# Kernel tuning notes

Hardware: AMD Instinct MI355X
Metric: run time of the kernel (lower is better)

Reference implementation:

```python
import jax, jax.numpy as jnp
import numpy as np

B, N, D, E = 64, 512, 256, 128   # batch, n_nodes, node_model_dim, edge_model_dim
N_ITERS = 20                      # max_iter_sinkhorn with fixed_n_iters=True


def setup_inputs() -> dict:
    key = jax.random.key(0)
    ks = jax.random.split(key, 9)
    return {
        "node_embeddings_inputs": jax.random.normal(ks[0], (B, N, D), jnp.float32),
        "node_masks_inputs": jax.random.randint(ks[1], (B, N), 0, 2).astype(bool),
        "node_embeddings_outputs": jax.random.normal(ks[2], (B, N, D), jnp.float32),
        # learned parameters
        "node_padding_features": jax.random.normal(ks[3], (1, 1, D), jnp.float32),
        "positional_encoding_outputs": jax.random.normal(ks[4], (1, N, D), jnp.float32),
        # stand-in for the (externally defined) EvoformerSetMatching pair stack:
        # a bilinear pair-affinity head, followed by the module's own linear_aff
        "W_a": jax.random.normal(ks[5], (D, E), jnp.float32) / np.sqrt(D),
        "W_b": jax.random.normal(ks[6], (D, E), jnp.float32) / np.sqrt(D),
        "w_aff": jax.random.normal(ks[7], (E,), jnp.float32) / np.sqrt(E),  # linear_aff weight
        "b_aff": jnp.zeros((), jnp.float32),                                # linear_aff bias
    }


def _sinkhorn(K, n_iters):
    # Fixed-iteration Sinkhorn projection toward a doubly-stochastic matrix:
    # alternately normalize columns (dim=2 sums) and rows (dim=1 sums).
    def step(P, _):
        P = P / jnp.sum(P, axis=2, keepdims=True)  # row-normalize over inputs axis
        P = P / jnp.sum(P, axis=1, keepdims=True)  # col-normalize over outputs axis
        return P, None
    P, _ = jax.lax.scan(step, K, None, length=n_iters)
    return P


def reference(node_embeddings_inputs, node_masks_inputs, node_embeddings_outputs,
              node_padding_features, positional_encoding_outputs,
              W_a, W_b, w_aff, b_aff):
    # replace padded input nodes with the learned padding feature
    mask = node_masks_inputs[..., None]                              # [B, N, 1]
    x_in = jnp.where(mask, node_padding_features, node_embeddings_inputs)
    # add positional encoding to output nodes (add_positionnal_outputs=True)
    x_out = node_embeddings_outputs + positional_encoding_outputs

    # pairwise affinity: aff[b, i(out), j(in)]  (linear_aff fused into the contraction
    # so the [B,N,N,E] pair tensor is never materialized)
    a = (x_out @ W_a) * w_aff                                        # [B, N, E]
    b = x_in @ W_b                                                   # [B, N, E]
    aff = jnp.einsum('bie,bje->bij', a, b) + b_aff                   # [B, N, N]

    # approximate doubly-stochastic init: average of the two marginal softmaxes
    K = 0.5 * jax.nn.softmax(aff, axis=1) + 0.5 * jax.nn.softmax(aff, axis=2)
    return _sinkhorn(K, N_ITERS)
```

## Files before the change

### kernel.cpp

```cpp
#include <hip/hip_runtime.h>
#include <cstddef>

static constexpr int CB = 64;
static constexpr int CN = 512;
static constexpr int CD = 256;
static constexpr int CE = 128;
static constexpr int CIT = 20;

typedef _Float16 half_t;
typedef __attribute__((ext_vector_type(8))) _Float16 v8h;
typedef __attribute__((ext_vector_type(4))) _Float16 v4h;
typedef __attribute__((ext_vector_type(4))) float v4f;

__device__ __forceinline__ void llc_store4(v4f* p, v4f v) {
  asm volatile("global_store_dwordx4 %0, %1, off sc0 sc1"
               :: "v"(p), "v"(v) : "memory");
}
__device__ __forceinline__ void llc_load3x4(const v4f* p0, const v4f* p1,
                                            const v4f* p2,
                                            v4f& a, v4f& b, v4f& c) {
  asm volatile("global_load_dwordx4 %0, %3, off sc0 sc1\n\t"
               "global_load_dwordx4 %1, %4, off sc0 sc1\n\t"
               "global_load_dwordx4 %2, %5, off sc0 sc1\n\t"
               "s_waitcnt vmcnt(0)"
               : "=&v"(a), "=&v"(b), "=&v"(c)
               : "v"(p0), "v"(p1), "v"(p2)
               : "memory");
}

__global__ __launch_bounds__(512) void k0_init(
    const void* __restrict__ mask, int* __restrict__ flag,
    const float* __restrict__ W_a, const float* __restrict__ W_b,
    const float* __restrict__ w_aff,
    half_t* __restrict__ WaF, half_t* __restrict__ WbF,
    float4* __restrict__ clearp, int nclear4) {
  const int tid = threadIdx.x;
  const int blk = blockIdx.x;
  if (blk == 1) return;
  if (blk >= 18) {
    const int idx = (blk - 18) * 512 + tid;
    if (idx < nclear4)
      clearp[idx] = make_float4(-1.0f, -1.0f, -1.0f, -1.0f);
    return;
  }
  if (blk >= 2) {
    const bool is_a = (blk < 10);
    const float* W = is_a ? W_a : W_b;
    half_t* WF = is_a ? WaF : WbF;
    const int e = (blk - (is_a ? 2 : 10)) * 512 + tid;
    const int fB = e >> 6, lane = e & 63;
    const int nn = fB >> 3, kf = fB & 7;
    const int col = nn * 16 + (lane & 15);
    const int q = lane >> 4;
    const float scale = is_a ? w_aff[col] : 1.0f;
    v8h hv;
#pragma unroll
    for (int j = 0; j < 8; ++j) {
      const int k = kf * 32 + q * 8 + j;
      hv[j] = (half_t)(W[(size_t)k * CE + col] * scale);
    }
    *(v8h*)&WF[(size_t)e * 8] = hv;
    return;
  }
  __shared__ int cnt[5];
  if (tid < 5) cnt[tid] = 0;
  __syncthreads();
  const unsigned char* p = (const unsigned char*)mask;
  int l0 = 0, l1 = 0, l2 = 0, l3 = 0, l4 = 0;
  const int base = tid * 64;
  for (int k = 0; k < 64; ++k) {
    const int off = base + k;
    if (p[off]) {
      const int m4 = off & 3;
      if (m4 == 1) l1++;
      else if (m4 == 2) l2++;
      else if (m4 == 3) l3++;
      else if ((off & 7) == 4) l4++;
      else l0++;
    }
  }
  if (l0) atomicAdd(&cnt[0], 1);
  if (l1) atomicAdd(&cnt[1], 1);
  if (l2) atomicAdd(&cnt[2], 1);
  if (l3) atomicAdd(&cnt[3], 1);
  if (l4) atomicAdd(&cnt[4], 1);
  __syncthreads();
  if (tid == 0) {
    int f;
    if (cnt[1]) f = 1;
    else if (cnt[2] || cnt[3]) f = 2;
    else if (cnt[4]) f = 0;
    else if (cnt[0]) f = 3;
    else f = 1;
    *flag = f;
  }
}

__global__ __launch_bounds__(256) void prep_both(
    const float* __restrict__ out_emb, const float* __restrict__ pos,
    const float* __restrict__ in_emb, const float* __restrict__ pad,
    const void* __restrict__ maskp, const int* __restrict__ flagp,
    const half_t* __restrict__ WaF, const half_t* __restrict__ WbF,
    half_t* __restrict__ A_h, half_t* __restrict__ Bm_h) {
  __shared__ half_t Xs[64][264];
  const int tid = threadIdx.x;
  const int wv = tid >> 6, ln = tid & 63;
  const bool isA = blockIdx.x < 512;
  const int row0 = (isA ? blockIdx.x : blockIdx.x - 512) * 64;
  const float* X = isA ? out_emb : in_emb;
  const float* extra = isA ? pos : pad;
  const half_t* Wfrag = isA ? WaF : WbF;
  half_t* out = isA ? A_h : Bm_h;
  const int flag = isA ? 0 : *flagp;

#pragma unroll 4
  for (int it = 0; it < 16; ++it) {
    const int r = it * 4 + wv;
    const int row = row0 + r;
    const int c = ln * 4;
    float4 x4;
    if (isA) {
      x4 = *(const float4*)&X[(size_t)row * CD + c];
      const int i = row & (CN - 1);
      const float4 p4 = *(const float4*)&extra[(size_t)i * CD + c];
      x4.x += p4.x; x4.y += p4.y; x4.z += p4.z; x4.w += p4.w;
    } else {
      bool m;
      if (flag == 1)      m = ((const unsigned char*)maskp)[row] != 0;
      else if (flag == 2) m = ((const float*)maskp)[row] != 0.0f;
      else if (flag == 3) m = ((const long long*)maskp)[row] != 0;
      else                m = ((const int*)maskp)[row] != 0;
      if (m) x4 = *(const float4*)&extra[c];
      else   x4 = *(const float4*)&X[(size_t)row * CD + c];
    }
    v4h hv;
    hv[0] = (half_t)x4.x; hv[1] = (half_t)x4.y;
    hv[2] = (half_t)x4.z; hv[3] = (half_t)x4.w;
    *(v4h*)&Xs[r][c] = hv;
  }
  __syncthreads();

  const int q = ln >> 4, l = ln & 15;
  v8h af[8];
#pragma unroll
  for (int kf = 0; kf < 8; ++kf)
    af[kf] = *(v8h*)&Xs[wv * 16 + l][kf * 32 + q * 8];
  v4f acc[8] = {};
#pragma unroll
  for (int nn = 0; nn < 8; ++nn) {
    v8h bf[8];
#pragma unroll
    for (int kf = 0; kf < 8; ++kf)
      bf[kf] = *(const v8h*)&Wfrag[(size_t)((nn * 8 + kf) * 64 + ln) * 8];
#pragma unroll
    for (int kf = 0; kf < 8; ++kf)
      acc[nn] = __builtin_amdgcn_mfma_f32_16x16x32_f16(af[kf], bf[kf], acc[nn], 0, 0, 0);
  }
#pragma unroll
  for (int nn = 0; nn < 8; ++nn)
#pragma unroll
    for (int g = 0; g < 4; ++g) {
      const int row = row0 + wv * 16 + q * 4 + g;
      out[(size_t)row * CE + nn * 16 + l] = (half_t)acc[nn][g];
    }
}

__global__ __launch_bounds__(512, 2) void fused_reg(
    const half_t* __restrict__ A_h, const half_t* __restrict__ B_h,
    const float* __restrict__ baff, float* __restrict__ P,
    float* __restrict__ partInit, float* __restrict__ partIter) {
  __shared__ float comb2[8][512][2];
  __shared__ __align__(16) float2 w12[512];
  __shared__ __align__(16) float QsL[512];
  __shared__ __align__(16) v4f csinv4[128];
  __shared__ half_t w1h[512];
  __shared__ half_t w2h[512];

  const int tid = threadIdx.x;
  const int wv = tid >> 6, ln = tid & 63;
  const int q = ln >> 4, l = ln & 15;
  const int b = blockIdx.x & 63;
  const int slab = blockIdx.x >> 6;
  const int i0 = slab * 128;
  const float bbs = *baff - 2.7725887f;

  int rs3[3];
  {
    int k = 0;
#pragma unroll
    for (int sl = 0; sl < 4; ++sl)
      if (sl != slab) rs3[k++] = sl;
  }

  v8h af[4];
  {
    const half_t* Arow = &A_h[((size_t)b * CN + i0 + wv * 16 + l) * CE];
#pragma unroll
    for (int ki = 0; ki < 4; ++ki)
      af[ki] = *(const v8h*)&Arow[ki * 32 + q * 8];
  }
  v4h eh[32];
  v4h ehT[32];
  const half_t* Bbase = &B_h[(size_t)b * CN * CE];
#pragma unroll
  for (int ct = 0; ct < 32; ++ct) {
    v8h bf[4];
    const half_t* Brow = &Bbase[(size_t)(ct * 16 + l) * CE];
#pragma unroll
    for (int ki = 0; ki < 4; ++ki)
      bf[ki] = *(const v8h*)&Brow[ki * 32 + q * 8];
    v4f acc = {}, accT = {};
#pragma unroll
    for (int ki = 0; ki < 4; ++ki) {
      acc  = __builtin_amdgcn_mfma_f32_16x16x32_f16(af[ki], bf[ki], acc,  0, 0, 0);
      accT = __builtin_amdgcn_mfma_f32_16x16x32_f16(bf[ki], af[ki], accT, 0, 0, 0);
    }
#pragma unroll
    for (int g = 0; g < 4; ++g) {
      eh[ct][g]  = (half_t)__expf(acc[g]  + bbs);
      ehT[ct][g] = (half_t)__expf(accT[g] + bbs);
    }
  }

  v4h ones;
  ones[0] = (half_t)1.0f; ones[1] = (half_t)1.0f;
  ones[2] = (half_t)1.0f; ones[3] = (half_t)1.0f;
  v4f rowacc0 = {}, rowacc1 = {};
#pragma unroll
  for (int ct = 0; ct < 32; ct += 2) {
    const v4f c0 = __builtin_amdgcn_mfma_f32_16x16x16f16(ones, eh[ct], (v4f){}, 0, 0, 0);
    const v4f c1 = __builtin_amdgcn_mfma_f32_16x16x16f16(ones, eh[ct + 1], (v4f){}, 0, 0, 0);
    if (ln < 16) {
      comb2[wv][ct * 16 + ln][0] = c0[0];
      comb2[wv][(ct + 1) * 16 + ln][0] = c1[0];
    }
    rowacc0 = __builtin_amdgcn_mfma_f32_16x16x16f16(ones, ehT[ct],     rowacc0, 0, 0, 0);
    rowacc1 = __builtin_amdgcn_mfma_f32_16x16x16f16(ones, ehT[ct + 1], rowacc1, 0, 0, 0);
  }
  const float rowtot = rowacc0[0] + rowacc1[0];
  float rv[4];
#pragma unroll
  for (int g = 0; g < 4; ++g)
    rv[g] = 1.0f / __shfl(rowtot, q * 4 + g);
  __syncthreads();

  {
    float S = 0.0f;
#pragma unroll
    for (int w = 0; w < 8; ++w) S += comb2[w][tid][0];
    QsL[tid] = S;
  }
  __syncthreads();
  if (tid < 128) {
    const v4f s4 = *(const v4f*)&QsL[tid * 4];
    v4f* pi4 = (v4f*)partInit + (size_t)b * 4 * 128;
    llc_store4(&pi4[slab * 128 + tid], s4);
    const v4f* q0 = &pi4[rs3[0] * 128 + tid];
    const v4f* q1 = &pi4[rs3[1] * 128 + tid];
    const v4f* q2 = &pi4[rs3[2] * 128 + tid];
    v4f r0, r1, r2;
    while (true) {
      llc_load3x4(q0, q1, q2, r0, r1, r2);
      if (r0[0] > 0.0f && r0[1] > 0.0f && r0[2] > 0.0f && r0[3] > 0.0f &&
          r1[0] > 0.0f && r1[1] > 0.0f && r1[2] > 0.0f && r1[3] > 0.0f &&
          r2[0] > 0.0f && r2[1] > 0.0f && r2[2] > 0.0f && r2[3] > 0.0f)
        break;
      __builtin_amdgcn_s_sleep(1);
    }
    const v4f T = s4 + r0 + r1 + r2;
    v4f ci;
    v4h w1v, w2v;
#pragma unroll
    for (int j = 0; j < 4; ++j) {
      ci[j] = 1.0f / T[j];
      w1v[j] = (half_t)(0.5f * ci[j]);
      w2v[j] = (half_t)1.0f;
    }
    csinv4[tid] = ci;
    *(v4h*)&w1h[tid * 4] = w1v;
    *(v4h*)&w2h[tid * 4] = w2v;
  }
  __syncthreads();
  const float ci0 = ((const float*)csinv4)[tid];

  const half_t* wbase = (l == 1) ? w2h : w1h;
  float u_[4], uri[4];
  for (int t = 0; t < CIT; ++t) {
    __syncthreads();
    v4f Pe = {}, Po = {};
#pragma unroll
    for (int ct = 0; ct < 32; ct += 2) {
      const v4h wf0 = *(const v4h*)&wbase[ct * 16 + q * 4];
      const v4h wf1 = *(const v4h*)&wbase[(ct + 1) * 16 + q * 4];
      Pe = __builtin_amdgcn_mfma_f32_16x16x16f16(wf0, ehT[ct],     Pe, 0, 0, 0);
      Po = __builtin_amdgcn_mfma_f32_16x16x16f16(wf1, ehT[ct + 1], Po, 0, 0, 0);
    }
    const float Prow1 = Pe[0] + Po[0];
    const float Prow2 = Pe[1] + Po[1];
    v4h u_h, uri_h;
#pragma unroll
    for (int g = 0; g < 4; ++g) {
      const float p1 = __shfl(Prow1, q * 4 + g);
      const float p2 = __shfl(Prow2, q * 4 + g);
      u_[g] = 1.0f / (p1 + 0.5f * rv[g] * p2);
      uri[g] = u_[g] * rv[g];
      u_h[g] = (half_t)u_[g];
      uri_h[g] = (half_t)uri[g];
    }
    const v4h a2 = (l == 1) ? uri_h : u_h;
#pragma unroll
    for (int ct = 0; ct < 32; ++ct) {
      const v4f s = __builtin_amdgcn_mfma_f32_16x16x16f16(a2, eh[ct], (v4f){}, 0, 0, 0);
      if (ln < 16)
        *(float2*)&comb2[wv][ct * 16 + ln][0] = make_float2(s[0], s[1]);
    }
    __syncthreads();
    {
      float S1 = 0.0f, S2 = 0.0f;
#pragma unroll
      for (int w = 0; w < 8; ++w) {
        const float2 c2v = *(const float2*)&comb2[w][tid][0];
        S1 += c2v.x;
        S2 += c2v.y;
      }
      QsL[tid] = 0.5f * fmaf(ci0, S1, S2);
    }
    __syncthreads();
    if (tid < 128) {
      const v4f Q4 = *(const v4f*)&QsL[tid * 4];
      v4f* pr4 = (v4f*)partIter + (((size_t)t * 64 + b) * 4) * 128;
      llc_store4(&pr4[slab * 128 + tid], Q4);
      const v4f* q0 = &pr4[rs3[0] * 128 + tid];
      const v4f* q1 = &pr4[rs3[1] * 128 + tid];
      const v4f* q2 = &pr4[rs3[2] * 128 + tid];
      v4f r0, r1, r2;
      while (true) {
        llc_load3x4(q0, q1, q2, r0, r1, r2);
        if (r0[0] > 0.0f && r0[1] > 0.0f && r0[2] > 0.0f && r0[3] > 0.0f &&
            r1[0] > 0.0f && r1[1] > 0.0f && r1[2] > 0.0f && r1[3] > 0.0f &&
            r2[0] > 0.0f && r2[1] > 0.0f && r2[2] > 0.0f && r2[3] > 0.0f)
          break;
        __builtin_amdgcn_s_sleep(1);
      }
      const v4f tot = Q4 + r0 + r1 + r2;
      const v4f ci = csinv4[tid];
      v4h w1v, w2v;
#pragma unroll
      for (int j = 0; j < 4; ++j) {
        const float vv = 1.0f / tot[j];
        w1v[j] = (half_t)(0.5f * vv * ci[j]);
        w2v[j] = (half_t)vv;
        if (t == CIT - 1)
          w12[tid * 4 + j] = make_float2(0.5f * vv * ci[j], vv);
      }
      *(v4h*)&w1h[tid * 4] = w1v;
      *(v4h*)&w2h[tid * 4] = w2v;
    }
  }

  __syncthreads();
  float* Pb = &P[((size_t)b * CN + i0 + wv * 16 + q * 4) * CN];
#pragma unroll
  for (int ct = 0; ct < 32; ++ct) {
    const float2 w = w12[ct * 16 + l];
    const float c1 = w.x;
    const float c2 = 0.5f * w.y;
#pragma unroll
    for (int g = 0; g < 4; ++g) {
      const float e = (float)eh[ct][g];
      Pb[(size_t)g * CN + ct * 16 + l] = e * fmaf(u_[g], c1, uri[g] * c2);
    }
  }
}

extern "C" void kernel_launch(void* const* d_in, const int* in_sizes, int n_in,
                              void* d_out, int out_size, void* d_ws, size_t ws_size,
                              hipStream_t stream) {
  const float* in_emb  = (const float*)d_in[0];
  const void*  mask    = d_in[1];
  const float* out_emb = (const float*)d_in[2];
  const float* pad     = (const float*)d_in[3];
  const float* pos     = (const float*)d_in[4];
  const float* W_a     = (const float*)d_in[5];
  const float* W_b     = (const float*)d_in[6];
  const float* w_aff   = (const float*)d_in[7];
  const float* b_aff   = (const float*)d_in[8];
  float* P = (float*)d_out;

  char* ws = (char*)d_ws;
  const size_t MB = 1024 * 1024;
  half_t* A_h  = (half_t*)ws;
  half_t* Bm_h = (half_t*)(ws + 8 * MB);
  int*    flag = (int*)(ws + 16 * MB);
  half_t* WaF  = (half_t*)(ws + 16 * MB + 16384);
  half_t* WbF  = (half_t*)(ws + 16 * MB + 16384 + 65536);
  float* partInit = (float*)(ws + 16 * MB + 256 * 1024);
  float* partIter = (float*)(ws + 16 * MB + 768 * 1024);

  const int nclear4 = (512 * 1024 + 10 * 1024 * 1024) / 16;
  const int nclrblk = (nclear4 + 511) / 512;

  k0_init<<<dim3(18 + nclrblk), dim3(512), 0, stream>>>(
      mask, flag, W_a, W_b, w_aff, WaF, WbF, (float4*)partInit, nclear4);
  prep_both<<<dim3(1024), dim3(256), 0, stream>>>(
      out_emb, pos, in_emb, pad, mask, flag, WaF, WbF, A_h, Bm_h);
  fused_reg<<<dim3(256), dim3(512), 0, stream>>>(
      A_h, Bm_h, b_aff, P, partInit, partIter);
}
```

Baseline: 308.2 us.

## Fuse input projection prep into the Sinkhorn kernel with cross-block marker sync

Removes the separate prep_both launch. Each block of the main kernel now projects its own slab of output nodes to A fragments through an LDS bounce, so A never goes to global memory. It also projects its slab of input nodes to B and publishes that slab to global memory with LLC-coherent stores. Blocks then spin on per-batch markers until the other three slabs of B are ready. This saves a kernel launch and the A round trip through global memory, at the cost of a cross-block spin barrier and projection work serialized in front of the affinity stage within only 256 blocks.

New measurement: 306.2 us. About the same (-0.6%).

```diff
diff --git a/kernel.cpp b/kernel.cpp
--- a/kernel.cpp
+++ b/kernel.cpp
@@ -14,6 +14,10 @@
 
 __device__ __forceinline__ void llc_store4(v4f* p, v4f v) {
   asm volatile("global_store_dwordx4 %0, %1, off sc0 sc1"
+               :: "v"(p), "v"(v) : "memory");
+}
+__device__ __forceinline__ void llc_storef(float* p, float v) {
+  asm volatile("global_store_dword %0, %1, off sc0 sc1"
                :: "v"(p), "v"(v) : "memory");
 }
 __device__ __forceinline__ void llc_load3x4(const v4f* p0, const v4f* p1,
@@ -26,6 +30,20 @@
                : "=&v"(a), "=&v"(b), "=&v"(c)
                : "v"(p0), "v"(p1), "v"(p2)
                : "memory");
+}
+__device__ __forceinline__ void llc_load3f(const float* p0, const float* p1,
+                                           const float* p2,
+                                           float& a, float& b, float& c) {
+  asm volatile("global_load_dword %0, %3, off sc0 sc1\n\t"
+               "global_load_dword %1, %4, off sc0 sc1\n\t"
+               "global_load_dword %2, %5, off sc0 sc1\n\t"
+               "s_waitcnt vmcnt(0)"
+               : "=&v"(a), "=&v"(b), "=&v"(c)
+               : "v"(p0), "v"(p1), "v"(p2)
+               : "memory");
+}
+__device__ __forceinline__ bool allpos(v4f v) {
+  return v[0] > 0.0f && v[1] > 0.0f && v[2] > 0.0f && v[3] > 0.0f;
 }
 
 __global__ __launch_bounds__(512) void k0_init(
@@ -96,85 +114,22 @@
   }
 }
 
-__global__ __launch_bounds__(256) void prep_both(
+__global__ __launch_bounds__(512, 2) void mega(
     const float* __restrict__ out_emb, const float* __restrict__ pos,
     const float* __restrict__ in_emb, const float* __restrict__ pad,
     const void* __restrict__ maskp, const int* __restrict__ flagp,
     const half_t* __restrict__ WaF, const half_t* __restrict__ WbF,
-    half_t* __restrict__ A_h, half_t* __restrict__ Bm_h) {
-  __shared__ half_t Xs[64][264];
-  const int tid = threadIdx.x;
-  const int wv = tid >> 6, ln = tid & 63;
-  const bool isA = blockIdx.x < 512;
-  const int row0 = (isA ? blockIdx.x : blockIdx.x - 512) * 64;
-  const float* X = isA ? out_emb : in_emb;
-  const float* extra = isA ? pos : pad;
-  const half_t* Wfrag = isA ? WaF : WbF;
-  half_t* out = isA ? A_h : Bm_h;
-  const int flag = isA ? 0 : *flagp;
-
-#pragma unroll 4
-  for (int it = 0; it < 16; ++it) {
-    const int r = it * 4 + wv;
-    const int row = row0 + r;
-    const int c = ln * 4;
-    float4 x4;
-    if (isA) {
-      x4 = *(const float4*)&X[(size_t)row * CD + c];
-      const int i = row & (CN - 1);
-      const float4 p4 = *(const float4*)&extra[(size_t)i * CD + c];
-      x4.x += p4.x; x4.y += p4.y; x4.z += p4.z; x4.w += p4.w;
-    } else {
-      bool m;
-      if (flag == 1)      m = ((const unsigned char*)maskp)[row] != 0;
-      else if (flag == 2) m = ((const float*)maskp)[row] != 0.0f;
-      else if (flag == 3) m = ((const long long*)maskp)[row] != 0;
-      else                m = ((const int*)maskp)[row] != 0;
-      if (m) x4 = *(const float4*)&extra[c];
-      else   x4 = *(const float4*)&X[(size_t)row * CD + c];
-    }
-    v4h hv;
-    hv[0] = (half_t)x4.x; hv[1] = (half_t)x4.y;
-    hv[2] = (half_t)x4.z; hv[3] = (half_t)x4.w;
-    *(v4h*)&Xs[r][c] = hv;
-  }
-  __syncthreads();
-
-  const int q = ln >> 4, l = ln & 15;
-  v8h af[8];
-#pragma unroll
-  for (int kf = 0; kf < 8; ++kf)
-    af[kf] = *(v8h*)&Xs[wv * 16 + l][kf * 32 + q * 8];
-  v4f acc[8] = {};
-#pragma unroll
-  for (int nn = 0; nn < 8; ++nn) {
-    v8h bf[8];
-#pragma unroll
-    for (int kf = 0; kf < 8; ++kf)
-      bf[kf] = *(const v8h*)&Wfrag[(size_t)((nn * 8 + kf) * 64 + ln) * 8];
-#pragma unroll
-    for (int kf = 0; kf < 8; ++kf)
-      acc[nn] = __builtin_amdgcn_mfma_f32_16x16x32_f16(af[kf], bf[kf], acc[nn], 0, 0, 0);
-  }
-#pragma unroll
-  for (int nn = 0; nn < 8; ++nn)
-#pragma unroll
-    for (int g = 0; g < 4; ++g) {
-      const int row = row0 + wv * 16 + q * 4 + g;
-      out[(size_t)row * CE + nn * 16 + l] = (half_t)acc[nn][g];
-    }
-}
-
-__global__ __launch_bounds__(512, 2) void fused_reg(
-    const half_t* __restrict__ A_h, const half_t* __restrict__ B_h,
+    half_t* __restrict__ Bm_h,
     const float* __restrict__ baff, float* __restrict__ P,
-    float* __restrict__ partInit, float* __restrict__ partIter) {
-  __shared__ float comb2[8][512][2];
+    float* __restrict__ partInit, float* __restrict__ partIter,
+    float* __restrict__ markers) {
+  __shared__ __align__(16) char smem2[34816];
   __shared__ __align__(16) float2 w12[512];
   __shared__ __align__(16) float QsL[512];
   __shared__ __align__(16) v4f csinv4[128];
-  __shared__ half_t w1h[512];
-  __shared__ half_t w2h[512];
+  __shared__ __align__(16) half_t wAll[1056];
+  half_t* bounce = (half_t*)smem2;
+  float (*comb2)[512][2] = (float (*)[512][2])smem2;
 
   const int tid = threadIdx.x;
   const int wv = tid >> 6, ln = tid & 63;
@@ -194,31 +149,133 @@
 
   v8h af[4];
   {
-    const half_t* Arow = &A_h[((size_t)b * CN + i0 + wv * 16 + l) * CE];
-#pragma unroll
-    for (int ki = 0; ki < 4; ++ki)
-      af[ki] = *(const v8h*)&Arow[ki * 32 + q * 8];
-  }
+    const int row = wv * 16 + l;
+    const size_t xr = ((size_t)b * CN + i0 + row) * CD;
+    const size_t pr = (size_t)(i0 + row) * CD;
+    v8h xf[8];
+#pragma unroll
+    for (int kf = 0; kf < 8; ++kf) {
+      const int c = kf * 32 + q * 8;
+      float4 a0 = *(const float4*)&out_emb[xr + c];
+      float4 a1 = *(const float4*)&out_emb[xr + c + 4];
+      const float4 p0 = *(const float4*)&pos[pr + c];
+      const float4 p1 = *(const float4*)&pos[pr + c + 4];
+      a0.x += p0.x; a0.y += p0.y; a0.z += p0.z; a0.w += p0.w;
+      a1.x += p1.x; a1.y += p1.y; a1.z += p1.z; a1.w += p1.w;
+      v8h h;
+      h[0] = (half_t)a0.x; h[1] = (half_t)a0.y;
+      h[2] = (half_t)a0.z; h[3] = (half_t)a0.w;
+      h[4] = (half_t)a1.x; h[5] = (half_t)a1.y;
+      h[6] = (half_t)a1.z; h[7] = (half_t)a1.w;
+      xf[kf] = h;
+    }
+    v4f acc[8] = {};
+#pragma unroll
+    for (int nn = 0; nn < 8; ++nn)
+#pragma unroll
+      for (int kf = 0; kf < 8; ++kf) {
+        const v8h bw = *(const v8h*)&WaF[(size_t)((nn * 8 + kf) * 64 + ln) * 8];
+        acc[nn] = __builtin_amdgcn_mfma_f32_16x16x32_f16(xf[kf], bw, acc[nn], 0, 0, 0);
+      }
+#pragma unroll
+    for (int nn = 0; nn < 8; ++nn)
+#pragma unroll
+      for (int g = 0; g < 4; ++g)
+        bounce[(size_t)(wv * 16 + q * 4 + g) * 136 + nn * 16 + l] = (half_t)acc[nn][g];
+  }
+  __syncthreads();
+#pragma unroll
+  for (int ki = 0; ki < 4; ++ki)
+    af[ki] = *(const v8h*)&bounce[(size_t)(wv * 16 + l) * 136 + ki * 32 + q * 8];
+  __syncthreads();
+
+  {
+    const int flag = *flagp;
+    const int row = wv * 16 + l;
+    const int grow = b * CN + i0 + row;
+    bool m;
+    if (flag == 1)      m = ((const unsigned char*)maskp)[grow] != 0;
+    else if (flag == 2) m = ((const float*)maskp)[grow] != 0.0f;
+    else if (flag == 3) m = ((const long long*)maskp)[grow] != 0;
+    else                m = ((const int*)maskp)[grow] != 0;
+    const size_t xr = (size_t)grow * CD;
+    v8h xf[8];
+#pragma unroll
+    for (int kf = 0; kf < 8; ++kf) {
+      const int c = kf * 32 + q * 8;
+      float4 a0, a1;
+      if (m) {
+        a0 = *(const float4*)&pad[c];
+        a1 = *(const float4*)&pad[c + 4];
+      } else {
+        a0 = *(const float4*)&in_emb[xr + c];
+        a1 = *(const float4*)&in_emb[xr + c + 4];
+      }
+      v8h h;
+      h[0] = (half_t)a0.x; h[1] = (half_t)a0.y;
+      h[2] = (half_t)a0.z; h[3] = (half_t)a0.w;
+      h[4] = (half_t)a1.x; h[5] = (half_t)a1.y;
+      h[6] = (half_t)a1.z; h[7] = (half_t)a1.w;
+      xf[kf] = h;
+    }
+    v4f acc[8] = {};
+#pragma unroll
+    for (int nn = 0; nn < 8; ++nn)
+#pragma unroll
+      for (int kf = 0; kf < 8; ++kf) {
+        const v8h bw = *(const v8h*)&WbF[(size_t)((nn * 8 + kf) * 64 + ln) * 8];
+        acc[nn] = __builtin_amdgcn_mfma_f32_16x16x32_f16(xf[kf], bw, acc[nn], 0, 0, 0);
+      }
+#pragma unroll
+    for (int nn = 0; nn < 8; ++nn)
+#pragma unroll
+      for (int g = 0; g < 4; ++g)
+        bounce[(size_t)(wv * 16 + q * 4 + g) * 136 + nn * 16 + l] = (half_t)acc[nn][g];
+  }
+  __syncthreads();
+  {
+    const int row = tid >> 2, qt = tid & 3;
+    half_t* dst = &Bm_h[((size_t)b * CN + i0 + row) * CE + qt * 32];
+    const half_t* src = &bounce[(size_t)row * 136 + qt * 32];
+#pragma unroll
+    for (int j = 0; j < 4; ++j)
+      llc_store4((v4f*)&dst[j * 8], *(const v4f*)&src[j * 8]);
+  }
+  __syncthreads();
+  if (tid == 0) llc_storef(&markers[(size_t)b * 4 + slab], 1.0f);
+
+  {
+    const float* mk = &markers[(size_t)b * 4];
+    float m0, m1, m2;
+    while (true) {
+      llc_load3f(&mk[rs3[0]], &mk[rs3[1]], &mk[rs3[2]], m0, m1, m2);
+      if (m0 > 0.0f && m1 > 0.0f && m2 > 0.0f) break;
+      __builtin_amdgcn_s_sleep(1);
+    }
+  }
+
   v4h eh[32];
   v4h ehT[32];
-  const half_t* Bbase = &B_h[(size_t)b * CN * CE];
-#pragma unroll
-  for (int ct = 0; ct < 32; ++ct) {
-    v8h bf[4];
-    const half_t* Brow = &Bbase[(size_t)(ct * 16 + l) * CE];
-#pragma unroll
-    for (int ki = 0; ki < 4; ++ki)
-      bf[ki] = *(const v8h*)&Brow[ki * 32 + q * 8];
-    v4f acc = {}, accT = {};
-#pragma unroll
-    for (int ki = 0; ki < 4; ++ki) {
-      acc  = __builtin_amdgcn_mfma_f32_16x16x32_f16(af[ki], bf[ki], acc,  0, 0, 0);
-      accT = __builtin_amdgcn_mfma_f32_16x16x32_f16(bf[ki], af[ki], accT, 0, 0, 0);
-    }
-#pragma unroll
-    for (int g = 0; g < 4; ++g) {
-      eh[ct][g]  = (half_t)__expf(acc[g]  + bbs);
-      ehT[ct][g] = (half_t)__expf(accT[g] + bbs);
+  {
+    const half_t* Bbase = &Bm_h[(size_t)b * CN * CE];
+#pragma unroll
+    for (int ct = 0; ct < 32; ++ct) {
+      v8h bf[4];
+      const half_t* Brow = &Bbase[(size_t)(ct * 16 + l) * CE];
+#pragma unroll
+      for (int ki = 0; ki < 4; ++ki)
+        bf[ki] = *(const v8h*)&Brow[ki * 32 + q * 8];
+      v4f acc = {}, accT = {};
+#pragma unroll
+      for (int ki = 0; ki < 4; ++ki) {
+        acc  = __builtin_amdgcn_mfma_f32_16x16x32_f16(af[ki], bf[ki], acc,  0, 0, 0);
+        accT = __builtin_amdgcn_mfma_f32_16x16x32_f16(bf[ki], af[ki], accT, 0, 0, 0);
+      }
+#pragma unroll
+      for (int g = 0; g < 4; ++g) {
+        eh[ct][g]  = (half_t)__expf(acc[g]  + bbs);
+        ehT[ct][g] = (half_t)__expf(accT[g] + bbs);
+      }
     }
   }
 
@@ -261,10 +318,7 @@
     v4f r0, r1, r2;
     while (true) {
       llc_load3x4(q0, q1, q2, r0, r1, r2);
-      if (r0[0] > 0.0f && r0[1] > 0.0f && r0[2] > 0.0f && r0[3] > 0.0f &&
-          r1[0] > 0.0f && r1[1] > 0.0f && r1[2] > 0.0f && r1[3] > 0.0f &&
-          r2[0] > 0.0f && r2[1] > 0.0f && r2[2] > 0.0f && r2[3] > 0.0f)
-        break;
+      if (allpos(r0) && allpos(r1) && allpos(r2)) break;
       __builtin_amdgcn_s_sleep(1);
     }
     const v4f T = s4 + r0 + r1 + r2;
@@ -277,13 +331,13 @@
       w2v[j] = (half_t)1.0f;
     }
     csinv4[tid] = ci;
-    *(v4h*)&w1h[tid * 4] = w1v;
-    *(v4h*)&w2h[tid * 4] = w2v;
+    *(v4h*)&wAll[tid * 4] = w1v;
+    *(v4h*)&wAll[544 + tid * 4] = w2v;
   }
   __syncthreads();
   const float ci0 = ((const float*)csinv4)[tid];
 
-  const half_t* wbase = (l == 1) ? w2h : w1h;
+  const half_t* wbase = (l == 1) ? (wAll + 544) : wAll;
   float u_[4], uri[4];
   for (int t = 0; t < CIT; ++t) {
     __syncthreads();
@@ -336,10 +390,7 @@
       v4f r0, r1, r2;
       while (true) {
         llc_load3x4(q0, q1, q2, r0, r1, r2);
-        if (r0[0] > 0.0f && r0[1] > 0.0f && r0[2] > 0.0f && r0[3] > 0.0f &&
-            r1[0] > 0.0f && r1[1] > 0.0f && r1[2] > 0.0f && r1[3] > 0.0f &&
-            r2[0] > 0.0f && r2[1] > 0.0f && r2[2] > 0.0f && r2[3] > 0.0f)
-          break;
+        if (allpos(r0) && allpos(r1) && allpos(r2)) break;
         __builtin_amdgcn_s_sleep(1);
       }
       const v4f tot = Q4 + r0 + r1 + r2;
@@ -353,8 +404,8 @@
         if (t == CIT - 1)
           w12[tid * 4 + j] = make_float2(0.5f * vv * ci[j], vv);
       }
-      *(v4h*)&w1h[tid * 4] = w1v;
-      *(v4h*)&w2h[tid * 4] = w2v;
+      *(v4h*)&wAll[tid * 4] = w1v;
+      *(v4h*)&wAll[544 + tid * 4] = w2v;
     }
   }
 
@@ -389,21 +440,21 @@
 
   char* ws = (char*)d_ws;
   const size_t MB = 1024 * 1024;
-  half_t* A_h  = (half_t*)ws;
-  half_t* Bm_h = (half_t*)(ws + 8 * MB);
-  int*    flag = (int*)(ws + 16 * MB);
-  half_t* WaF  = (half_t*)(ws + 16 * MB + 16384);
-  half_t* WbF  = (half_t*)(ws + 16 * MB + 16384 + 65536);
-  float* partInit = (float*)(ws + 16 * MB + 256 * 1024);
-  float* partIter = (float*)(ws + 16 * MB + 768 * 1024);
-
-  const int nclear4 = (512 * 1024 + 10 * 1024 * 1024) / 16;
+  const size_t KB = 1024;
+  half_t* Bm_h = (half_t*)ws;
+  int*    flag = (int*)(ws + 8 * MB);
+  half_t* WaF  = (half_t*)(ws + 8 * MB + 16 * KB);
+  half_t* WbF  = (half_t*)(ws + 8 * MB + 80 * KB);
+  float* partInit = (float*)(ws + 9 * MB);
+  float* partIter = (float*)(ws + 9 * MB + 512 * KB);
+  float* markers  = (float*)(ws + 9 * MB + 512 * KB + 10 * MB);
+
+  const int nclear4 = (512 * 1024 + 10 * 1024 * 1024 + 1024) / 16;
   const int nclrblk = (nclear4 + 511) / 512;
 
   k0_init<<<dim3(18 + nclrblk), dim3(512), 0, stream>>>(
       mask, flag, W_a, W_b, w_aff, WaF, WbF, (float4*)partInit, nclear4);
-  prep_both<<<dim3(1024), dim3(256), 0, stream>>>(
-      out_emb, pos, in_emb, pad, mask, flag, WaF, WbF, A_h, Bm_h);
-  fused_reg<<<dim3(256), dim3(512), 0, stream>>>(
-      A_h, Bm_h, b_aff, P, partInit, partIter);
-}
+  mega<<<dim3(256), dim3(512), 0, stream>>>(
+      out_emb, pos, in_emb, pad, mask, flag, WaF, WbF, Bm_h,
+      b_aff, P, partInit, partIter, markers);
+}
```
